# Optimization experiments

Measured on AMD Instinct MI355X. Metric: run time of the kernel, lower is better.

The kernel has to match this reference:

```python
import jax, jax.numpy as jnp
import numpy as np

T, N, C = 1024, 4, 4
RADIUS, COMPRESSION = 256, 1
TAU = 2.0  # LIF filter time constant (LIF_Filter source unavailable; exponential leaky integrator assumed)


def _build_delay():
    # Mirrors JeffressFilter.__init__ delay construction exactly.
    neg = np.arange(-RADIUS, 0, COMPRESSION, dtype=np.int64)
    pos = np.arange(RADIUS, 0, -COMPRESSION, dtype=np.int64)[::-1]
    _d = np.concatenate([neg, pos]).reshape(-1, 1)            # (D_out, 1)
    delay = np.maximum(np.concatenate([_d, -_d], axis=1), 0)  # relu -> (D_out, 2)
    return jnp.asarray(delay, dtype=jnp.int32)


def setup_inputs() -> dict:
    key = jax.random.key(0)
    k1, k2 = jax.random.split(key)
    x = jax.random.normal(k1, (T, N, C, 2), dtype=jnp.float32)
    delay = _build_delay()                                   # (D_out, 2) int
    d_out = delay.shape[0]                                   # 512
    # get_weight(1.0, 10.0, compression) source unavailable; stand-in float vector per output channel
    weight = jax.random.normal(k2, (d_out,), dtype=jnp.float32)
    return {"x": x, "weight": weight, "delay": delay}


def _lif_filter(x):
    # Leaky integrator over time axis 0: v[t] = exp(-1/tau) * v[t-1] + x[t]
    decay = jnp.asarray(np.exp(-1.0 / TAU), dtype=x.dtype)

    def step(v, xt):
        v = decay * v + xt
        return v, v

    _, y = jax.lax.scan(step, jnp.zeros(x.shape[1:], x.dtype), x)
    return y  # (T, N, C, 2)


def reference(x, weight, delay):
    Tlen = x.shape[0]
    y = _lif_filter(x)                                       # (T, N, C, 2)

    t = jnp.arange(Tlen, dtype=jnp.int32)
    # SpikeDelay.forward: mask rows t >= T - delay to 0, then gather at (t - delay) % T.
    # Equivalent post-gather: out[t] = y[t - delay] if t >= delay else 0 (zero-padded shift).
    t_idx = (t[:, None, None] - delay[None]) % Tlen          # (T, D_out, 2)
    i_idx = jnp.arange(2, dtype=jnp.int32)[None, None, :]    # broadcast over (T, D_out, 2)
    yt = jnp.moveaxis(y, -1, 1)                              # (T, 2, N, C)
    gathered = yt[t_idx, i_idx]                              # (T, D_out, 2, N, C)
    mask = t[:, None, None] >= delay[None]                   # (T, D_out, 2)
    out = jnp.where(mask[..., None, None], gathered, 0.0)
    out = out.sum(axis=2)                                    # sum over in_features=2 -> (T, D_out, N, C)
    out = jnp.moveaxis(out, 1, -1)                           # (T, N, C, D_out)
    return out * weight                                      # scale per output channel
```

## Files before the change

### kernel.cpp

```cpp
#include <hip/hip_runtime.h>


#define T_LEN  1024
#define D_OUT  512
#define NC     16
#define PAD    256
#define ROW    (PAD + T_LEN)
#define YB_OFF (NC * ROW)

__global__ __launch_bounds__(64) void lif_scan_kernel(const float* __restrict__ x,
                                                      float* __restrict__ ws) {
    const int tid = threadIdx.x;
    const int b   = blockIdx.x;

    #pragma unroll
    for (int k = 0; k < 8; ++k) {
        const int id = (b * 64 + tid) * 8 + k;
        const int r  = id >> 8;
        const int c  = id & 255;
        ws[r * ROW + c] = 0.0f;
    }

    if (tid < 32) {
        const int ch = tid;
        const int nc = ch >> 1;
        const int i  = ch & 1;
        float* row = ws + (i ? YB_OFF : 0) + nc * ROW + PAD;

        const int   t0    = b * 64;
        const float decay = 0.60653065971263342f;

        float v = 0.0f;
        #pragma unroll 8
        for (int k = 0; k < 64; ++k) {
            const int t = t0 - 64 + k;
            const float xv = (t >= 0) ? x[t * 32 + ch] : 0.0f;
            v = decay * v + xv;
        }
        #pragma unroll 8
        for (int k = 0; k < 64; ++k) {
            const int t = t0 + k;
            v = decay * v + x[t * 32 + ch];
            row[t] = v;
        }
    }
}

__global__ __launch_bounds__(256) void jeffress_kernel(const float* __restrict__ ws,
                                                       const float* __restrict__ w,
                                                       const int* __restrict__ delay,
                                                       float4* __restrict__ out) {
    const int bid = blockIdx.x;
    const int nc  = bid & 15;
    const int t0  = (bid >> 4) * 16 + (threadIdx.x >> 7) * 8;
    const int d4  = threadIdx.x & 127;
    const int d   = d4 * 4;

    const int4*   dp  = (const int4*)(delay + 2 * d);
    const int4    e01 = dp[0];
    const int4    e23 = dp[1];
    const float4  wv  = ((const float4*)w)[d4];

    const float* A = ws + nc * ROW + PAD + t0;
    const float* B = ws + YB_OFF + nc * ROW + PAD + t0;
    const float* a0 = A - e01.x;  const float* b0 = B - e01.y;
    const float* a1 = A - e01.z;  const float* b1 = B - e01.w;
    const float* a2 = A - e23.x;  const float* b2 = B - e23.y;
    const float* a3 = A - e23.z;  const float* b3 = B - e23.w;

    float4* op = out + (size_t)t0 * (NC * D_OUT / 4) + nc * (D_OUT / 4) + d4;

    #pragma unroll
    for (int j = 0; j < 8; ++j) {
        float4 o;
        o.x = wv.x * (a0[j] + b0[j]);
        o.y = wv.y * (a1[j] + b1[j]);
        o.z = wv.z * (a2[j] + b2[j]);
        o.w = wv.w * (a3[j] + b3[j]);
        op[j * (NC * D_OUT / 4)] = o;
    }
}

extern "C" void kernel_launch(void* const* d_in, const int* in_sizes, int n_in,
                              void* d_out, int out_size, void* d_ws, size_t ws_size,
                              hipStream_t stream) {
    const float* x      = (const float*)d_in[0];
    const float* weight = (const float*)d_in[1];
    const int*   delay  = (const int*)d_in[2];
    float* out = (float*)d_out;
    float* ws  = (float*)d_ws;

    lif_scan_kernel<<<16, 64, 0, stream>>>(x, ws);

    const int nblocks = (T_LEN / 16) * NC;
    jeffress_kernel<<<nblocks, 256, 0, stream>>>(ws, weight, delay, (float4*)out);
}
```

Measured before the change: 78.66 us.

## Remap jeffress kernel to one delay channel per thread with scalar stores

```diff
diff --git a/kernel.cpp b/kernel.cpp
--- a/kernel.cpp
+++ b/kernel.cpp
@@ -49,35 +49,27 @@
 __global__ __launch_bounds__(256) void jeffress_kernel(const float* __restrict__ ws,
                                                        const float* __restrict__ w,
                                                        const int* __restrict__ delay,
-                                                       float4* __restrict__ out) {
-    const int bid = blockIdx.x;
-    const int nc  = bid & 15;
-    const int t0  = (bid >> 4) * 16 + (threadIdx.x >> 7) * 8;
-    const int d4  = threadIdx.x & 127;
-    const int d   = d4 * 4;
+                                                       float* __restrict__ out) {
+    const int bid  = blockIdx.x;
+    const int d0   = (bid & 7) * 64;
+    const int nc   = (bid >> 3) & 15;
+    const int t0   = (bid >> 7) * 16;
+    const int lane = threadIdx.x & 63;
+    const int wv   = threadIdx.x >> 6;
+    const int d    = d0 + lane;
+    const int tb   = t0 + wv * 4;
 
-    const int4*   dp  = (const int4*)(delay + 2 * d);
-    const int4    e01 = dp[0];
-    const int4    e23 = dp[1];
-    const float4  wv  = ((const float4*)w)[d4];
+    const int2  dl = ((const int2*)delay)[d];
+    const float wd = w[d];
 
-    const float* A = ws + nc * ROW + PAD + t0;
-    const float* B = ws + YB_OFF + nc * ROW + PAD + t0;
-    const float* a0 = A - e01.x;  const float* b0 = B - e01.y;
-    const float* a1 = A - e01.z;  const float* b1 = B - e01.w;
-    const float* a2 = A - e23.x;  const float* b2 = B - e23.y;
-    const float* a3 = A - e23.z;  const float* b3 = B - e23.w;
+    const float* pA = ws + nc * ROW + PAD + tb - dl.x;
+    const float* pB = ws + YB_OFF + nc * ROW + PAD + tb - dl.y;
 
-    float4* op = out + (size_t)t0 * (NC * D_OUT / 4) + nc * (D_OUT / 4) + d4;
+    float* op = out + (size_t)tb * (NC * D_OUT) + nc * D_OUT + d;
 
     #pragma unroll
-    for (int j = 0; j < 8; ++j) {
-        float4 o;
-        o.x = wv.x * (a0[j] + b0[j]);
-        o.y = wv.y * (a1[j] + b1[j]);
-        o.z = wv.z * (a2[j] + b2[j]);
-        o.w = wv.w * (a3[j] + b3[j]);
-        op[j * (NC * D_OUT / 4)] = o;
+    for (int j = 0; j < 4; ++j) {
+        op[j * (NC * D_OUT)] = wd * (pA[j] + pB[j]);
     }
 }
 
@@ -92,6 +84,5 @@
 
     lif_scan_kernel<<<16, 64, 0, stream>>>(x, ws);
 
-    const int nblocks = (T_LEN / 16) * NC;
-    jeffress_kernel<<<nblocks, 256, 0, stream>>>(ws, weight, delay, (float4*)out);
+    jeffress_kernel<<<8192, 256, 0, stream>>>(ws, weight, delay, out);
 }
```

Result: slower. 80.31 us (+2.1%).
